# Optimization experiments

Measured on AMD Instinct MI355X. Metric: run time of the kernel, lower is better.

Reference implementation:

```python
import jax, jax.numpy as jnp
import numpy as np

N, NI, NF, NE, B, K, KD = 200000, 64, 128, 256, 16, 27, 8
ND = N // 8
EPS = 1e-5


def setup_inputs() -> dict:
    key = jax.random.key(0)
    ks = jax.random.split(key, 12)
    s = lambda i, shape: jax.random.normal(ks[i], shape, jnp.float32) * 0.02
    x = jax.random.normal(ks[0], (N, NI), jnp.float32)
    t = jax.random.normal(ks[1], (B, NE), jnp.float32)
    b_idx = jax.random.randint(ks[2], (N,), 0, B)
    nbr = jax.random.randint(ks[3], (K, N), 0, N)
    nbr = jnp.where(jax.random.uniform(ks[4], (K, N)) < 0.3, -1, nbr)
    nbr_down = jax.random.randint(ks[5], (KD, ND), 0, N)
    return dict(
        x=x, t=t, b_idx=b_idx, nbr=nbr, nbr_down=nbr_down,
        g1=jnp.ones((NI,), jnp.float32), be1=jnp.zeros((NI,), jnp.float32),
        W1=s(6, (K, NI, NF)), b1=jnp.zeros((NF,), jnp.float32),
        Wt=s(7, (NE, 2 * NF)), bt=jnp.zeros((2 * NF,), jnp.float32),
        g2=jnp.ones((NF,), jnp.float32), be2=jnp.zeros((NF,), jnp.float32),
        W2=s(8, (K, NF, NF)), b2=jnp.zeros((NF,), jnp.float32),
        Wid=s(9, (NI, NF)), bid=jnp.zeros((NF,), jnp.float32),
        Wd=s(10, (KD, NF, NF)),
    )


def bn_silu(x, g, b):
    # spnn.BatchNorm (training batch stats over voxels) + spnn.SiLU
    m = x.mean(0)
    v = x.var(0)
    return jax.nn.silu((x - m) * jax.lax.rsqrt(v + EPS) * g + b)


def sparse_conv(x, W, nbr):
    # gather-matmul-accumulate over kernel offsets; nbr[k] == -1 -> no neighbor
    def body(acc, kv):
        Wk, nk = kv
        xg = jnp.where((nk >= 0)[:, None], x[jnp.clip(nk, 0)], 0.0)  # [M, Ci]
        return acc + xg @ Wk, None
    out0 = jnp.zeros((nbr.shape[1], W.shape[-1]), x.dtype)
    out, _ = jax.lax.scan(body, out0, (W, nbr))
    return out


def reference(x, t, b_idx, nbr, nbr_down, g1, be1, W1, b1, Wt, bt,
              g2, be2, W2, b2, Wid, bid, Wd):
    # EmbResBlock
    h = sparse_conv(bn_silu(x, g1, be1), W1, nbr) + b1          # conv1 [N, NF]
    tp = jax.nn.silu(t) @ Wt + bt                                # proj_mlp [B, 2*NF]
    scale, shift = jnp.split(tp, 2, axis=-1)
    # TimeEmbeddingBlock: one edge per node -> gather + affine
    h = (1.0 + scale[b_idx]) * h + shift[b_idx]
    h = sparse_conv(bn_silu(h, g2, be2), W2, nbr) + b2           # conv2 [N, NF]
    h = h + x @ Wid + bid                                        # idconv residual
    # strided down conv (ks=2, stride=2, no bias) -> [ND, NF]
    return sparse_conv(h, Wd, nbr_down)
```

## Files before the change

kernel.cpp:

```cpp
#include <hip/hip_runtime.h>

#define NV 200000
#define NDN 25000
#define EPSV 1e-5f

typedef short bf16x8 __attribute__((ext_vector_type(8)));
typedef float f32x16 __attribute__((ext_vector_type(16)));

static __device__ __forceinline__ float silu_f(float v) { return v / (1.0f + __expf(-v)); }
static __device__ __forceinline__ unsigned short f2b(float f) {
    unsigned u = __float_as_uint(f);
    return (unsigned short)((u + 0x7FFFu + ((u >> 16) & 1u)) >> 16);
}
static __device__ __forceinline__ float b2f(unsigned short h) {
    return __uint_as_float(((unsigned)h) << 16);
}
static __device__ __forceinline__ bf16x8 bc8(uint4 v) { return __builtin_bit_cast(bf16x8, v); }
#define MFMA32(a, b, c) __builtin_amdgcn_mfma_f32_32x32x16_bf16(a, b, c, 0, 0, 0)

static __device__ __forceinline__ void gload_lds16(const uint4* g, uint4* l) {
    __builtin_amdgcn_global_load_lds((const __attribute__((address_space(1))) unsigned*)(g),
                                     (__attribute__((address_space(3))) unsigned*)(l), 16, 0, 0);
}

#define OFF_STATS1 0
#define OFF_STATS2 512
#define OFF_TP     4096
#define OFF_W1B    32768
#define OFF_W2B    (OFF_W1B + 27 * 64 * 128 * 2)
#define OFF_WDB    (OFF_W2B + 27 * 128 * 128 * 2)
#define OFF_WIDB   (OFF_WDB + 8 * 128 * 128 * 2)
#define OFF_H1     (2u << 20)
#define OFF_H2     (28u << 20)
#define OFF_H4     (80u << 20)


__global__ void k_zero(float* p) {
    int i = threadIdx.x;
    if (i < 384) p[i] = 0.0f;
}

__global__ __launch_bounds__(256) void k_stats1(const float* __restrict__ x,
                                                float* __restrict__ stats) {
    int c = threadIdx.x & 63;
    int r0 = blockIdx.x * 4 + (threadIdx.x >> 6);
    float s = 0.f, q = 0.f;
    for (int r = r0; r < NV; r += gridDim.x * 4) {
        float v = x[r * 64 + c];
        s += v; q += v * v;
    }
    __shared__ float rs[256], rq[256];
    rs[threadIdx.x] = s; rq[threadIdx.x] = q;
    __syncthreads();
    if (threadIdx.x < 64) {
        s = rs[threadIdx.x] + rs[threadIdx.x + 64] + rs[threadIdx.x + 128] + rs[threadIdx.x + 192];
        q = rq[threadIdx.x] + rq[threadIdx.x + 64] + rq[threadIdx.x + 128] + rq[threadIdx.x + 192];
        atomicAdd(&stats[c], s);
        atomicAdd(&stats[64 + c], q);
    }
}

__global__ __launch_bounds__(256) void k_tp(const float* __restrict__ t,
                                            const float* __restrict__ Wt,
                                            const float* __restrict__ bt,
                                            float* __restrict__ tp) {
    __shared__ float st[256];
    int b = blockIdx.x, o = threadIdx.x;
    st[o] = silu_f(t[b * 256 + o]);
    __syncthreads();
    float acc = bt[o];
    for (int e = 0; e < 256; e++) acc += st[e] * Wt[e * 256 + o];
    tp[b * 256 + o] = acc;
}

__global__ __launch_bounds__(256) void k_swz(const float* __restrict__ W, uint4* __restrict__ dst,
                                             int Kc, int S) {
    int t = blockIdx.x * 256 + threadIdx.x;
    int total = Kc * S * 4 * 64;
    if (t >= total) return;
    int L = t & 63;
    int u = t >> 6;
    int nt = u & 3; u >>= 2;
    int s = u % S;
    int kk = u / S;
    int CI = S * 16;
    int c0 = s * 16 + (L >> 5) * 8;
    int f = nt * 32 + (L & 31);
    union { unsigned short e[8]; uint4 v; } uu;
#pragma unroll
    for (int j = 0; j < 8; j++) uu.e[j] = f2b(W[(kk * CI + c0 + j) * 128 + f]);
    dst[t] = uu.v;
}

__global__ __launch_bounds__(256) void k_h1(const float* __restrict__ x,
                                            const float* __restrict__ g1,
                                            const float* __restrict__ be1,
                                            const float* __restrict__ stats,
                                            unsigned short* __restrict__ H1) {
    int i = blockIdx.x * 256 + threadIdx.x;
    if (i >= NV * 16) return;
    int c4 = (i & 15) * 4;
    float4 v = ((const float4*)x)[i];
    float vv[4] = {v.x, v.y, v.z, v.w};
    ushort4 o;
    unsigned short os[4];
#pragma unroll
    for (int j = 0; j < 4; j++) {
        int c = c4 + j;
        float m = stats[c] * (1.0f / NV);
        float var = stats[64 + c] * (1.0f / NV) - m * m;
        float a = g1[c] * rsqrtf(var + EPSV);
        float b = be1[c] - m * a;
        os[j] = f2b(silu_f(vv[j] * a + b));
    }
    o.x = os[0]; o.y = os[1]; o.z = os[2]; o.w = os[3];
    ((ushort4*)H1)[i] = o;
}

__global__ __launch_bounds__(256) void k_h3(unsigned short* __restrict__ H,
                                            const float* __restrict__ g2,
                                            const float* __restrict__ be2,
                                            const float* __restrict__ stats2) {
    int i = blockIdx.x * 256 + threadIdx.x;
    if (i >= NV * 16) return;
    union { uint4 v; unsigned short e[8]; } uu;
    uu.v = ((const uint4*)H)[i];
    int f0 = (i & 15) * 8;
#pragma unroll
    for (int j = 0; j < 8; j++) {
        int f = f0 + j;
        float m = stats2[f] * (1.0f / NV);
        float var = stats2[128 + f] * (1.0f / NV) - m * m;
        float a = g2[f] * rsqrtf(var + EPSV);
        float b = be2[f] - m * a;
        uu.e[j] = f2b(silu_f(b2f(uu.e[j]) * a + b));
    }
    ((uint4*)H)[i] = uu.v;
}


#define C2_STEP(AC, AN, IDXC, IDXN, LDSC, LDSN, KK)                                    \
    {                                                                                  \
        if ((KK) + 1 < 27) {                                                           \
            const uint4* pn = (const uint4*)H3 + (long)(IDXC) * 16;                    \
            _Pragma("unroll")                                                          \
            for (int s = 0; s < 8; s++) {                                              \
                AN[s] = make_uint4(0, 0, 0, 0);                                        \
                if ((IDXC) >= 0) AN[s] = pn[s * 2 + h];                                \
            }                                                                          \
        }                                                                              \
        IDXN = ((KK) + 2 < 27 && row0 < NV) ? nbr[((KK) + 2) * NV + row0] : -1;        \
        if ((KK) + 1 < 27) {                                                           \
            const uint4* gsrc = W2b + ((KK) + 1) * 2048 + (w * 8) * 64 + lane;         \
            _Pragma("unroll")                                                          \
            for (int j = 0; j < 8; j++)                                                \
                gload_lds16(gsrc + j * 64, &sB[(LDSN) + (w * 8 + j) * 64]);            \
        }                                                                              \
        _Pragma("unroll")                                                              \
        for (int s = 0; s < 8; s++) {                                                  \
            uint4 b0 = sB[(LDSC) + (s * 4 + 0) * 64 + lane];                           \
            uint4 b1v = sB[(LDSC) + (s * 4 + 1) * 64 + lane];                          \
            uint4 b2v = sB[(LDSC) + (s * 4 + 2) * 64 + lane];                          \
            uint4 b3v = sB[(LDSC) + (s * 4 + 3) * 64 + lane];                          \
            acc[0] = MFMA32(bc8(AC[s]), bc8(b0), acc[0]);                              \
            acc[1] = MFMA32(bc8(AC[s]), bc8(b1v), acc[1]);                             \
            acc[2] = MFMA32(bc8(AC[s]), bc8(b2v), acc[2]);                             \
            acc[3] = MFMA32(bc8(AC[s]), bc8(b3v), acc[3]);                             \
        }                                                                              \
        __syncthreads();                                                               \
    }

#define C1_STEP(AC, AN, IDXC, IDXN, LDSC, LDSN, KK)                                    \
    {                                                                                  \
        if ((KK) + 1 < 27) {                                                           \
            const uint4* pn = (const uint4*)H1 + (long)(IDXC) * 8;                     \
            _Pragma("unroll")                                                          \
            for (int s = 0; s < 4; s++) {                                              \
                AN[s] = make_uint4(0, 0, 0, 0);                                        \
                if ((IDXC) >= 0) AN[s] = pn[s * 2 + h];                                \
            }                                                                          \
        }                                                                              \
        IDXN = ((KK) + 2 < 27 && row0 < NV) ? nbr[((KK) + 2) * NV + row0] : -1;        \
        if ((KK) + 1 < 27) {                                                           \
            const uint4* gsrc = W1b + ((KK) + 1) * 1024 + (w * 4) * 64 + lane;         \
            _Pragma("unroll")                                                          \
            for (int j = 0; j < 4; j++)                                                \
                gload_lds16(gsrc + j * 64, &sB[(LDSN) + (w * 4 + j) * 64]);            \
        }                                                                              \
        _Pragma("unroll")                                                              \
        for (int s = 0; s < 4; s++) {                                                  \
            uint4 b0 = sB[(LDSC) + (s * 4 + 0) * 64 + lane];                           \
            uint4 b1v = sB[(LDSC) + (s * 4 + 1) * 64 + lane];                          \
            uint4 b2v = sB[(LDSC) + (s * 4 + 2) * 64 + lane];                          \
            uint4 b3v = sB[(LDSC) + (s * 4 + 3) * 64 + lane];                          \
            acc[0] = MFMA32(bc8(AC[s]), bc8(b0), acc[0]);                              \
            acc[1] = MFMA32(bc8(AC[s]), bc8(b1v), acc[1]);                             \
            acc[2] = MFMA32(bc8(AC[s]), bc8(b2v), acc[2]);                             \
            acc[3] = MFMA32(bc8(AC[s]), bc8(b3v), acc[3]);                             \
        }                                                                              \
        __syncthreads();                                                               \
    }

#define CD_STEP(AC, AN, IDXC, IDXN, LDSC, LDSN, KK)                                    \
    {                                                                                  \
        if ((KK) + 1 < 8) {                                                            \
            const uint4* pn = (const uint4*)H4 + (long)(IDXC) * 16;                    \
            _Pragma("unroll")                                                          \
            for (int s = 0; s < 8; s++) AN[s] = pn[s * 2 + h];                         \
        }                                                                              \
        IDXN = ((KK) + 2 < 8 && row0 < NDN) ? nbrd[((KK) + 2) * NDN + row0] : 0;       \
        if ((KK) + 1 < 8) {                                                            \
            const uint4* gsrc = Wdb + ((KK) + 1) * 2048 + (w * 8) * 64 + lane;         \
            _Pragma("unroll")                                                          \
            for (int j = 0; j < 8; j++)                                                \
                gload_lds16(gsrc + j * 64, &sB[(LDSN) + (w * 8 + j) * 64]);            \
        }                                                                              \
        _Pragma("unroll")                                                              \
        for (int s = 0; s < 8; s++) {                                                  \
            uint4 b0 = sB[(LDSC) + (s * 4 + 0) * 64 + lane];                           \
            uint4 b1v = sB[(LDSC) + (s * 4 + 1) * 64 + lane];                          \
            uint4 b2v = sB[(LDSC) + (s * 4 + 2) * 64 + lane];                          \
            uint4 b3v = sB[(LDSC) + (s * 4 + 3) * 64 + lane];                          \
            acc[0] = MFMA32(bc8(AC[s]), bc8(b0), acc[0]);                              \
            acc[1] = MFMA32(bc8(AC[s]), bc8(b1v), acc[1]);                             \
            acc[2] = MFMA32(bc8(AC[s]), bc8(b2v), acc[2]);                             \
            acc[3] = MFMA32(bc8(AC[s]), bc8(b3v), acc[3]);                             \
        }                                                                              \
        __syncthreads();                                                               \
    }

__global__ __launch_bounds__(256, 2) void k_conv1(const unsigned short* __restrict__ H1,
                                                  const int* __restrict__ nbr,
                                                  const uint4* __restrict__ W1b,
                                                  const float* __restrict__ b1,
                                                  const int* __restrict__ b_idx,
                                                  const float* __restrict__ tp,
                                                  unsigned short* __restrict__ H2,
                                                  float* __restrict__ stats2) {
    extern __shared__ uint4 sB[];
    __shared__ float ssum[128], ssq[128];
    int tid = threadIdx.x;
    int w = tid >> 6, lane = tid & 63, m = lane & 31, h = lane >> 5;
    int n0 = blockIdx.x * 128;
    int row0 = n0 + w * 32 + m;
    if (tid < 128) { ssum[tid] = 0.f; ssq[tid] = 0.f; }
    f32x16 z;
#pragma unroll
    for (int r = 0; r < 16; r++) z[r] = 0.f;
    f32x16 acc[4] = {z, z, z, z};
    uint4 aA[4], aB[4];
    int idxE, idxO;

    {
        const uint4* g0 = W1b + (w * 4) * 64 + lane;
#pragma unroll
        for (int j = 0; j < 4; j++) gload_lds16(g0 + j * 64, &sB[(w * 4 + j) * 64]);
        int idx0 = (row0 < NV) ? nbr[row0] : -1;
        idxO = (row0 < NV) ? nbr[NV + row0] : -1;
        const uint4* p0 = (const uint4*)H1 + (long)idx0 * 8;
#pragma unroll
        for (int s = 0; s < 4; s++) {
            aA[s] = make_uint4(0, 0, 0, 0);
            if (idx0 >= 0) aA[s] = p0[s * 2 + h];
        }
        idxE = idx0;
        __syncthreads();
    }
    for (int k = 0; k < 27; k += 2) {
        C1_STEP(aA, aB, idxO, idxE, 0, 1024, k);
        if (k + 1 < 27) C1_STEP(aB, aA, idxE, idxO, 1024, 0, (k + 1));
    }

    int col = m;
    float b1f[4];
#pragma unroll
    for (int nt = 0; nt < 4; nt++) b1f[nt] = b1[nt * 32 + col];
    float sl[4] = {0.f, 0.f, 0.f, 0.f}, ql[4] = {0.f, 0.f, 0.f, 0.f};
#pragma unroll
    for (int r = 0; r < 16; r++) {
        int row = w * 32 + (r & 3) + 8 * (r >> 2) + 4 * h;
        int g = n0 + row;
        if (g < NV) {
            int b = b_idx[g];
            const float* tpb = tp + b * 256;
#pragma unroll
            for (int nt = 0; nt < 4; nt++) {
                int f = nt * 32 + col;
                float val = acc[nt][r] + b1f[nt];
                float h2v = (1.0f + tpb[f]) * val + tpb[128 + f];
                H2[(long)g * 128 + f] = f2b(h2v);
                sl[nt] += h2v; ql[nt] += h2v * h2v;
            }
        }
    }
#pragma unroll
    for (int nt = 0; nt < 4; nt++) {
        int f = nt * 32 + col;
        atomicAdd(&ssum[f], sl[nt]);
        atomicAdd(&ssq[f], ql[nt]);
    }
    __syncthreads();
    if (tid < 128) {
        atomicAdd(&stats2[tid], ssum[tid]);
        atomicAdd(&stats2[128 + tid], ssq[tid]);
    }
}

__global__ __launch_bounds__(256, 2) void k_conv2(const unsigned short* __restrict__ H3,
                                                  const int* __restrict__ nbr,
                                                  const uint4* __restrict__ W2b,
                                                  const float* __restrict__ b2,
                                                  const float* __restrict__ x,
                                                  const uint4* __restrict__ Widb,
                                                  const float* __restrict__ bid,
                                                  unsigned short* __restrict__ H4) {
    extern __shared__ uint4 sB[];
    int tid = threadIdx.x;
    int w = tid >> 6, lane = tid & 63, m = lane & 31, h = lane >> 5;
    int n0 = blockIdx.x * 128;
    int row0 = n0 + w * 32 + m;
    f32x16 z;
#pragma unroll
    for (int r = 0; r < 16; r++) z[r] = 0.f;
    f32x16 acc[4] = {z, z, z, z};
    uint4 aA[8], aB[8];
    int idxE, idxO;

    {
        const uint4* g0 = W2b + (w * 8) * 64 + lane;
#pragma unroll
        for (int j = 0; j < 8; j++) gload_lds16(g0 + j * 64, &sB[(w * 8 + j) * 64]);
        int idx0 = (row0 < NV) ? nbr[row0] : -1;
        idxO = (row0 < NV) ? nbr[NV + row0] : -1;
        const uint4* p0 = (const uint4*)H3 + (long)idx0 * 16;
#pragma unroll
        for (int s = 0; s < 8; s++) {
            aA[s] = make_uint4(0, 0, 0, 0);
            if (idx0 >= 0) aA[s] = p0[s * 2 + h];
        }
        idxE = idx0;
        __syncthreads();
    }
    for (int k = 0; k < 27; k += 2) {
        C2_STEP(aA, aB, idxO, idxE, 0, 2048, k);
        if (k + 1 < 27) C2_STEP(aB, aA, idxE, idxO, 2048, 0, (k + 1));
    }

    {
        uint4 a0[4];
#pragma unroll
        for (int s = 0; s < 4; s++) {
            union { unsigned short e[8]; uint4 v; } u0;
            u0.v = make_uint4(0, 0, 0, 0);
            if (row0 < NV) {
                const float4* xr = (const float4*)(x + (long)row0 * 64);
                float4 f0 = xr[s * 4 + h * 2], f1 = xr[s * 4 + h * 2 + 1];
                u0.e[0] = f2b(f0.x); u0.e[1] = f2b(f0.y); u0.e[2] = f2b(f0.z); u0.e[3] = f2b(f0.w);
                u0.e[4] = f2b(f1.x); u0.e[5] = f2b(f1.y); u0.e[6] = f2b(f1.z); u0.e[7] = f2b(f1.w);
            }
            a0[s] = u0.v;
        }
#pragma unroll
        for (int s = 0; s < 4; s++) {
#pragma unroll
            for (int nt = 0; nt < 4; nt++) {
                uint4 bv = Widb[(s * 4 + nt) * 64 + lane];
                acc[nt] = MFMA32(bc8(a0[s]), bc8(bv), acc[nt]);
            }
        }
    }
    int col = m;
#pragma unroll
    for (int nt = 0; nt < 4; nt++) {
        int f = nt * 32 + col;
        float bias = b2[f] + bid[f];
#pragma unroll
        for (int r = 0; r < 16; r++) {
            int row = w * 32 + (r & 3) + 8 * (r >> 2) + 4 * h;
            int g = n0 + row;
            if (g < NV) H4[(long)g * 128 + f] = f2b(acc[nt][r] + bias);
        }
    }
}

__global__ __launch_bounds__(256, 2) void k_down(const unsigned short* __restrict__ H4,
                                                 const int* __restrict__ nbrd,
                                                 const uint4* __restrict__ Wdb,
                                                 float* __restrict__ out) {
    extern __shared__ uint4 sB[];
    int tid = threadIdx.x;
    int w = tid >> 6, lane = tid & 63, m = lane & 31, h = lane >> 5;
    int n0 = blockIdx.x * 128;
    int row0 = n0 + w * 32 + m;
    f32x16 z;
#pragma unroll
    for (int r = 0; r < 16; r++) z[r] = 0.f;
    f32x16 acc[4] = {z, z, z, z};
    uint4 aA[8], aB[8];
    int idxE, idxO;

    {
        const uint4* g0 = Wdb + (w * 8) * 64 + lane;
#pragma unroll
        for (int j = 0; j < 8; j++) gload_lds16(g0 + j * 64, &sB[(w * 8 + j) * 64]);
        int idx0 = (row0 < NDN) ? nbrd[row0] : 0;
        idxO = (row0 < NDN) ? nbrd[NDN + row0] : 0;
        const uint4* p0 = (const uint4*)H4 + (long)idx0 * 16;
#pragma unroll
        for (int s = 0; s < 8; s++) aA[s] = p0[s * 2 + h];
        idxE = idx0;
        __syncthreads();
    }
    for (int k = 0; k < 8; k += 2) {
        CD_STEP(aA, aB, idxO, idxE, 0, 2048, k);
        CD_STEP(aB, aA, idxE, idxO, 2048, 0, (k + 1));
    }

    int col = m;
#pragma unroll
    for (int nt = 0; nt < 4; nt++) {
        int f = nt * 32 + col;
#pragma unroll
        for (int r = 0; r < 16; r++) {
            int row = w * 32 + (r & 3) + 8 * (r >> 2) + 4 * h;
            int g = n0 + row;
            if (g < NDN) out[(long)g * 128 + f] = acc[nt][r];
        }
    }
}


extern "C" void kernel_launch(void* const* d_in, const int* in_sizes, int n_in,
                              void* d_out, int out_size, void* d_ws, size_t ws_size,
                              hipStream_t stream) {
    const float* x   = (const float*)d_in[0];
    const float* t   = (const float*)d_in[1];
    const int* b_idx = (const int*)d_in[2];
    const int* nbr   = (const int*)d_in[3];
    const int* nbrd  = (const int*)d_in[4];
    const float* g1  = (const float*)d_in[5];
    const float* be1 = (const float*)d_in[6];
    const float* W1  = (const float*)d_in[7];
    const float* b1  = (const float*)d_in[8];
    const float* Wt  = (const float*)d_in[9];
    const float* bt  = (const float*)d_in[10];
    const float* g2  = (const float*)d_in[11];
    const float* be2 = (const float*)d_in[12];
    const float* W2  = (const float*)d_in[13];
    const float* b2  = (const float*)d_in[14];
    const float* Wid = (const float*)d_in[15];
    const float* bid = (const float*)d_in[16];
    const float* Wd  = (const float*)d_in[17];
    float* out = (float*)d_out;

    char* ws = (char*)d_ws;
    float* stats1 = (float*)(ws + OFF_STATS1);
    float* stats2 = (float*)(ws + OFF_STATS2);
    float* tp     = (float*)(ws + OFF_TP);
    uint4* W1b    = (uint4*)(ws + OFF_W1B);
    uint4* W2b    = (uint4*)(ws + OFF_W2B);
    uint4* Wdb    = (uint4*)(ws + OFF_WDB);
    uint4* Widb   = (uint4*)(ws + OFF_WIDB);
    unsigned short* H1 = (unsigned short*)(ws + OFF_H1);
    unsigned short* H2 = (unsigned short*)(ws + OFF_H2);
    unsigned short* H4 = (unsigned short*)(ws + OFF_H4);

    k_zero<<<1, 384, 0, stream>>>((float*)ws);
    k_stats1<<<400, 256, 0, stream>>>(x, stats1);
    k_tp<<<16, 256, 0, stream>>>(t, Wt, bt, tp);
    k_swz<<<108, 256, 0, stream>>>(W1, W1b, 27, 4);
    k_swz<<<216, 256, 0, stream>>>(W2, W2b, 27, 8);
    k_swz<<<64, 256, 0, stream>>>(Wd, Wdb, 8, 8);
    k_swz<<<4, 256, 0, stream>>>(Wid, Widb, 1, 4);
    k_h1<<<12500, 256, 0, stream>>>(x, g1, be1, stats1, H1);
    k_conv1<<<(NV + 127) / 128, 256, 2 * 1024 * 16, stream>>>(H1, nbr, W1b, b1, b_idx, tp, H2, stats2);
    k_h3<<<12500, 256, 0, stream>>>(H2, g2, be2, stats2);
    k_conv2<<<(NV + 127) / 128, 256, 2 * 2048 * 16, stream>>>(H2, nbr, W2b, b2, x, Widb, bid, H4);
    k_down<<<(NDN + 127) / 128, 256, 2 * 2048 * 16, stream>>>(H4, nbrd, Wdb, out);
}
```

Before: 680.8 us.

## Register-staged weight prefetch, zero-row gathers, and lighter barriers in sparse convs

```diff
diff --git a/kernel.cpp b/kernel.cpp
--- a/kernel.cpp
+++ b/kernel.cpp
@@ -17,11 +17,6 @@
 }
 static __device__ __forceinline__ bf16x8 bc8(uint4 v) { return __builtin_bit_cast(bf16x8, v); }
 #define MFMA32(a, b, c) __builtin_amdgcn_mfma_f32_32x32x16_bf16(a, b, c, 0, 0, 0)
-
-static __device__ __forceinline__ void gload_lds16(const uint4* g, uint4* l) {
-    __builtin_amdgcn_global_load_lds((const __attribute__((address_space(1))) unsigned*)(g),
-                                     (__attribute__((address_space(3))) unsigned*)(l), 16, 0, 0);
-}
 
 #define OFF_STATS1 0
 #define OFF_STATS2 512
@@ -38,6 +33,12 @@
 __global__ void k_zero(float* p) {
     int i = threadIdx.x;
     if (i < 384) p[i] = 0.0f;
+}
+
+__global__ void k_zrow(unsigned short* H1, unsigned short* H2) {
+    int t = threadIdx.x;
+    if (t < 64) H1[(long)NV * 64 + t] = 0;
+    H2[(long)NV * 128 + t] = 0;
 }
 
 __global__ __launch_bounds__(256) void k_stats1(const float* __restrict__ x,
@@ -142,20 +143,24 @@
 #define C2_STEP(AC, AN, IDXC, IDXN, LDSC, LDSN, KK)                                    \
     {                                                                                  \
         if ((KK) + 1 < 27) {                                                           \
-            const uint4* pn = (const uint4*)H3 + (long)(IDXC) * 16;                    \
-            _Pragma("unroll")                                                          \
-            for (int s = 0; s < 8; s++) {                                              \
-                AN[s] = make_uint4(0, 0, 0, 0);                                        \
-                if ((IDXC) >= 0) AN[s] = pn[s * 2 + h];                                \
-            }                                                                          \
-        }                                                                              \
-        IDXN = ((KK) + 2 < 27 && row0 < NV) ? nbr[((KK) + 2) * NV + row0] : -1;        \
-        if ((KK) + 1 < 27) {                                                           \
-            const uint4* gsrc = W2b + ((KK) + 1) * 2048 + (w * 8) * 64 + lane;         \
             _Pragma("unroll")                                                          \
             for (int j = 0; j < 8; j++)                                                \
-                gload_lds16(gsrc + j * 64, &sB[(LDSN) + (w * 8 + j) * 64]);            \
-        }                                                                              \
+                sB[(LDSN) + (w * 8 + j) * 64 + lane] = wR[j];                          \
+        }                                                                              \
+        __builtin_amdgcn_sched_barrier(0);                                             \
+        {                                                                              \
+            int rn_ = ((IDXC) < 0) ? NV : (IDXC);                                      \
+            const uint4* pn = (const uint4*)H3 + (long)rn_ * 16;                       \
+            _Pragma("unroll")                                                          \
+            for (int s = 0; s < 8; s++) AN[s] = pn[s * 2 + h];                         \
+        }                                                                              \
+        IDXN = nbr[((KK) + 2 < 27 ? (KK) + 2 : 26) * NV + row0c];                      \
+        if ((KK) + 2 < 27) {                                                           \
+            const uint4* gw = W2b + ((KK) + 2) * 2048 + (w * 8) * 64 + lane;           \
+            _Pragma("unroll")                                                          \
+            for (int j = 0; j < 8; j++) wR[j] = gw[j * 64];                            \
+        }                                                                              \
+        __builtin_amdgcn_sched_barrier(0);                                             \
         _Pragma("unroll")                                                              \
         for (int s = 0; s < 8; s++) {                                                  \
             uint4 b0 = sB[(LDSC) + (s * 4 + 0) * 64 + lane];                           \
@@ -167,26 +172,32 @@
             acc[2] = MFMA32(bc8(AC[s]), bc8(b2v), acc[2]);                             \
             acc[3] = MFMA32(bc8(AC[s]), bc8(b3v), acc[3]);                             \
         }                                                                              \
-        __syncthreads();                                                               \
+        asm volatile("s_waitcnt lgkmcnt(0)" ::: "memory");                             \
+        __builtin_amdgcn_s_barrier();                                                  \
+        __builtin_amdgcn_sched_barrier(0);                                             \
     }
 
 #define C1_STEP(AC, AN, IDXC, IDXN, LDSC, LDSN, KK)                                    \
     {                                                                                  \
         if ((KK) + 1 < 27) {                                                           \
-            const uint4* pn = (const uint4*)H1 + (long)(IDXC) * 8;                     \
-            _Pragma("unroll")                                                          \
-            for (int s = 0; s < 4; s++) {                                              \
-                AN[s] = make_uint4(0, 0, 0, 0);                                        \
-                if ((IDXC) >= 0) AN[s] = pn[s * 2 + h];                                \
-            }                                                                          \
-        }                                                                              \
-        IDXN = ((KK) + 2 < 27 && row0 < NV) ? nbr[((KK) + 2) * NV + row0] : -1;        \
-        if ((KK) + 1 < 27) {                                                           \
-            const uint4* gsrc = W1b + ((KK) + 1) * 1024 + (w * 4) * 64 + lane;         \
             _Pragma("unroll")                                                          \
             for (int j = 0; j < 4; j++)                                                \
-                gload_lds16(gsrc + j * 64, &sB[(LDSN) + (w * 4 + j) * 64]);            \
-        }                                                                              \
+                sB[(LDSN) + (w * 4 + j) * 64 + lane] = wR[j];                          \
+        }                                                                              \
+        __builtin_amdgcn_sched_barrier(0);                                             \
+        {                                                                              \
+            int rn_ = ((IDXC) < 0) ? NV : (IDXC);                                      \
+            const uint4* pn = (const uint4*)H1 + (long)rn_ * 8;                        \
+            _Pragma("unroll")                                                          \
+            for (int s = 0; s < 4; s++) AN[s] = pn[s * 2 + h];                         \
+        }                                                                              \
+        IDXN = nbr[((KK) + 2 < 27 ? (KK) + 2 : 26) * NV + row0c];                      \
+        if ((KK) + 2 < 27) {                                                           \
+            const uint4* gw = W1b + ((KK) + 2) * 1024 + (w * 4) * 64 + lane;           \
+            _Pragma("unroll")                                                          \
+            for (int j = 0; j < 4; j++) wR[j] = gw[j * 64];                            \
+        }                                                                              \
+        __builtin_amdgcn_sched_barrier(0);                                             \
         _Pragma("unroll")                                                              \
         for (int s = 0; s < 4; s++) {                                                  \
             uint4 b0 = sB[(LDSC) + (s * 4 + 0) * 64 + lane];                           \
@@ -198,23 +209,31 @@
             acc[2] = MFMA32(bc8(AC[s]), bc8(b2v), acc[2]);                             \
             acc[3] = MFMA32(bc8(AC[s]), bc8(b3v), acc[3]);                             \
         }                                                                              \
-        __syncthreads();                                                               \
+        asm volatile("s_waitcnt lgkmcnt(0)" ::: "memory");                             \
+        __builtin_amdgcn_s_barrier();                                                  \
+        __builtin_amdgcn_sched_barrier(0);                                             \
     }
 
 #define CD_STEP(AC, AN, IDXC, IDXN, LDSC, LDSN, KK)                                    \
     {                                                                                  \
         if ((KK) + 1 < 8) {                                                            \
+            _Pragma("unroll")                                                          \
+            for (int j = 0; j < 8; j++)                                                \
+                sB[(LDSN) + (w * 8 + j) * 64 + lane] = wR[j];                          \
+        }                                                                              \
+        __builtin_amdgcn_sched_barrier(0);                                             \
+        {                                                                              \
             const uint4* pn = (const uint4*)H4 + (long)(IDXC) * 16;                    \
             _Pragma("unroll")                                                          \
             for (int s = 0; s < 8; s++) AN[s] = pn[s * 2 + h];                         \
         }                                                                              \
-        IDXN = ((KK) + 2 < 8 && row0 < NDN) ? nbrd[((KK) + 2) * NDN + row0] : 0;       \
-        if ((KK) + 1 < 8) {                                                            \
-            const uint4* gsrc = Wdb + ((KK) + 1) * 2048 + (w * 8) * 64 + lane;         \
-            _Pragma("unroll")                                                          \
-            for (int j = 0; j < 8; j++)                                                \
-                gload_lds16(gsrc + j * 64, &sB[(LDSN) + (w * 8 + j) * 64]);            \
-        }                                                                              \
+        IDXN = nbrd[((KK) + 2 < 8 ? (KK) + 2 : 7) * NDN + row0c];                      \
+        if ((KK) + 2 < 8) {                                                            \
+            const uint4* gw = Wdb + ((KK) + 2) * 2048 + (w * 8) * 64 + lane;           \
+            _Pragma("unroll")                                                          \
+            for (int j = 0; j < 8; j++) wR[j] = gw[j * 64];                            \
+        }                                                                              \
+        __builtin_amdgcn_sched_barrier(0);                                             \
         _Pragma("unroll")                                                              \
         for (int s = 0; s < 8; s++) {                                                  \
             uint4 b0 = sB[(LDSC) + (s * 4 + 0) * 64 + lane];                           \
@@ -226,10 +245,12 @@
             acc[2] = MFMA32(bc8(AC[s]), bc8(b2v), acc[2]);                             \
             acc[3] = MFMA32(bc8(AC[s]), bc8(b3v), acc[3]);                             \
         }                                                                              \
-        __syncthreads();                                                               \
-    }
-
-__global__ __launch_bounds__(256, 2) void k_conv1(const unsigned short* __restrict__ H1,
+        asm volatile("s_waitcnt lgkmcnt(0)" ::: "memory");                             \
+        __builtin_amdgcn_s_barrier();                                                  \
+        __builtin_amdgcn_sched_barrier(0);                                             \
+    }
+
+__global__ __launch_bounds__(256, 3) void k_conv1(const unsigned short* __restrict__ H1,
                                                   const int* __restrict__ nbr,
                                                   const uint4* __restrict__ W1b,
                                                   const float* __restrict__ b1,
@@ -243,28 +264,33 @@
     int w = tid >> 6, lane = tid & 63, m = lane & 31, h = lane >> 5;
     int n0 = blockIdx.x * 128;
     int row0 = n0 + w * 32 + m;
+    int row0c = row0 < NV ? row0 : NV - 1;
     if (tid < 128) { ssum[tid] = 0.f; ssq[tid] = 0.f; }
     f32x16 z;
 #pragma unroll
     for (int r = 0; r < 16; r++) z[r] = 0.f;
     f32x16 acc[4] = {z, z, z, z};
-    uint4 aA[4], aB[4];
-    int idxE, idxO;
+    uint4 aA[4], aB[4], wR[4];
+    int idxE = 0, idxO;
 
     {
-        const uint4* g0 = W1b + (w * 4) * 64 + lane;
-#pragma unroll
-        for (int j = 0; j < 4; j++) gload_lds16(g0 + j * 64, &sB[(w * 4 + j) * 64]);
-        int idx0 = (row0 < NV) ? nbr[row0] : -1;
-        idxO = (row0 < NV) ? nbr[NV + row0] : -1;
-        const uint4* p0 = (const uint4*)H1 + (long)idx0 * 8;
-#pragma unroll
-        for (int s = 0; s < 4; s++) {
-            aA[s] = make_uint4(0, 0, 0, 0);
-            if (idx0 >= 0) aA[s] = p0[s * 2 + h];
-        }
-        idxE = idx0;
-        __syncthreads();
+        int idx0 = nbr[row0c];
+        idxO = nbr[NV + row0c];
+        const uint4* gw = W1b + (w * 4) * 64 + lane;
+#pragma unroll
+        for (int j = 0; j < 4; j++) wR[j] = gw[j * 64];
+        int rn_ = idx0 < 0 ? NV : idx0;
+        const uint4* p0 = (const uint4*)H1 + (long)rn_ * 8;
+#pragma unroll
+        for (int s = 0; s < 4; s++) aA[s] = p0[s * 2 + h];
+#pragma unroll
+        for (int j = 0; j < 4; j++) sB[(w * 4 + j) * 64 + lane] = wR[j];
+        const uint4* gw1 = W1b + 1024 + (w * 4) * 64 + lane;
+#pragma unroll
+        for (int j = 0; j < 4; j++) wR[j] = gw1[j * 64];
+        asm volatile("s_waitcnt lgkmcnt(0)" ::: "memory");
+        __builtin_amdgcn_s_barrier();
+        __builtin_amdgcn_sched_barrier(0);
     }
     for (int k = 0; k < 27; k += 2) {
         C1_STEP(aA, aB, idxO, idxE, 0, 1024, k);
@@ -319,27 +345,32 @@
     int w = tid >> 6, lane = tid & 63, m = lane & 31, h = lane >> 5;
     int n0 = blockIdx.x * 128;
     int row0 = n0 + w * 32 + m;
+    int row0c = row0 < NV ? row0 : NV - 1;
     f32x16 z;
 #pragma unroll
     for (int r = 0; r < 16; r++) z[r] = 0.f;
     f32x16 acc[4] = {z, z, z, z};
-    uint4 aA[8], aB[8];
-    int idxE, idxO;
+    uint4 aA[8], aB[8], wR[8];
+    int idxE = 0, idxO;
 
     {
-        const uint4* g0 = W2b + (w * 8) * 64 + lane;
-#pragma unroll
-        for (int j = 0; j < 8; j++) gload_lds16(g0 + j * 64, &sB[(w * 8 + j) * 64]);
-        int idx0 = (row0 < NV) ? nbr[row0] : -1;
-        idxO = (row0 < NV) ? nbr[NV + row0] : -1;
-        const uint4* p0 = (const uint4*)H3 + (long)idx0 * 16;
-#pragma unroll
-        for (int s = 0; s < 8; s++) {
-            aA[s] = make_uint4(0, 0, 0, 0);
-            if (idx0 >= 0) aA[s] = p0[s * 2 + h];
-        }
-        idxE = idx0;
-        __syncthreads();
+        int idx0 = nbr[row0c];
+        idxO = nbr[NV + row0c];
+        const uint4* gw = W2b + (w * 8) * 64 + lane;
+#pragma unroll
+        for (int j = 0; j < 8; j++) wR[j] = gw[j * 64];
+        int rn_ = idx0 < 0 ? NV : idx0;
+        const uint4* p0 = (const uint4*)H3 + (long)rn_ * 16;
+#pragma unroll
+        for (int s = 0; s < 8; s++) aA[s] = p0[s * 2 + h];
+#pragma unroll
+        for (int j = 0; j < 8; j++) sB[(w * 8 + j) * 64 + lane] = wR[j];
+        const uint4* gw1 = W2b + 2048 + (w * 8) * 64 + lane;
+#pragma unroll
+        for (int j = 0; j < 8; j++) wR[j] = gw1[j * 64];
+        asm volatile("s_waitcnt lgkmcnt(0)" ::: "memory");
+        __builtin_amdgcn_s_barrier();
+        __builtin_amdgcn_sched_barrier(0);
     }
     for (int k = 0; k < 27; k += 2) {
         C2_STEP(aA, aB, idxO, idxE, 0, 2048, k);
@@ -392,24 +423,31 @@
     int w = tid >> 6, lane = tid & 63, m = lane & 31, h = lane >> 5;
     int n0 = blockIdx.x * 128;
     int row0 = n0 + w * 32 + m;
+    int row0c = row0 < NDN ? row0 : NDN - 1;
     f32x16 z;
 #pragma unroll
     for (int r = 0; r < 16; r++) z[r] = 0.f;
     f32x16 acc[4] = {z, z, z, z};
-    uint4 aA[8], aB[8];
-    int idxE, idxO;
+    uint4 aA[8], aB[8], wR[8];
+    int idxE = 0, idxO;
 
     {
-        const uint4* g0 = Wdb + (w * 8) * 64 + lane;
-#pragma unroll
-        for (int j = 0; j < 8; j++) gload_lds16(g0 + j * 64, &sB[(w * 8 + j) * 64]);
-        int idx0 = (row0 < NDN) ? nbrd[row0] : 0;
-        idxO = (row0 < NDN) ? nbrd[NDN + row0] : 0;
+        int idx0 = nbrd[row0c];
+        idxO = nbrd[NDN + row0c];
+        const uint4* gw = Wdb + (w * 8) * 64 + lane;
+#pragma unroll
+        for (int j = 0; j < 8; j++) wR[j] = gw[j * 64];
         const uint4* p0 = (const uint4*)H4 + (long)idx0 * 16;
 #pragma unroll
         for (int s = 0; s < 8; s++) aA[s] = p0[s * 2 + h];
-        idxE = idx0;
-        __syncthreads();
+#pragma unroll
+        for (int j = 0; j < 8; j++) sB[(w * 8 + j) * 64 + lane] = wR[j];
+        const uint4* gw1 = Wdb + 2048 + (w * 8) * 64 + lane;
+#pragma unroll
+        for (int j = 0; j < 8; j++) wR[j] = gw1[j * 64];
+        asm volatile("s_waitcnt lgkmcnt(0)" ::: "memory");
+        __builtin_amdgcn_s_barrier();
+        __builtin_amdgcn_sched_barrier(0);
     }
     for (int k = 0; k < 8; k += 2) {
         CD_STEP(aA, aB, idxO, idxE, 0, 2048, k);
@@ -466,6 +504,7 @@
     unsigned short* H4 = (unsigned short*)(ws + OFF_H4);
 
     k_zero<<<1, 384, 0, stream>>>((float*)ws);
+    k_zrow<<<1, 128, 0, stream>>>(H1, H2);
     k_stats1<<<400, 256, 0, stream>>>(x, stats1);
     k_tp<<<16, 256, 0, stream>>>(t, Wt, bt, tp);
     k_swz<<<108, 256, 0, stream>>>(W1, W1b, 27, 4);
```

New measurement: 1.238 ms. 1.82x slower.

## Read conv weights directly from global memory instead of staging through LDS

Applied to the files above, without the earlier changes.

```diff
diff --git a/kernel.cpp b/kernel.cpp
--- a/kernel.cpp
+++ b/kernel.cpp
@@ -17,11 +17,6 @@
 }
 static __device__ __forceinline__ bf16x8 bc8(uint4 v) { return __builtin_bit_cast(bf16x8, v); }
 #define MFMA32(a, b, c) __builtin_amdgcn_mfma_f32_32x32x16_bf16(a, b, c, 0, 0, 0)
-
-static __device__ __forceinline__ void gload_lds16(const uint4* g, uint4* l) {
-    __builtin_amdgcn_global_load_lds((const __attribute__((address_space(1))) unsigned*)(g),
-                                     (__attribute__((address_space(3))) unsigned*)(l), 16, 0, 0);
-}
 
 #define OFF_STATS1 0
 #define OFF_STATS2 512
@@ -139,7 +134,7 @@
 }
 
 
-#define C2_STEP(AC, AN, IDXC, IDXN, LDSC, LDSN, KK)                                    \
+#define C2_STEP(AC, AN, IDXC, IDXN, KK)                                                \
     {                                                                                  \
         if ((KK) + 1 < 27) {                                                           \
             const uint4* pn = (const uint4*)H3 + (long)(IDXC) * 16;                    \
@@ -150,27 +145,21 @@
             }                                                                          \
         }                                                                              \
         IDXN = ((KK) + 2 < 27 && row0 < NV) ? nbr[((KK) + 2) * NV + row0] : -1;        \
-        if ((KK) + 1 < 27) {                                                           \
-            const uint4* gsrc = W2b + ((KK) + 1) * 2048 + (w * 8) * 64 + lane;         \
-            _Pragma("unroll")                                                          \
-            for (int j = 0; j < 8; j++)                                                \
-                gload_lds16(gsrc + j * 64, &sB[(LDSN) + (w * 8 + j) * 64]);            \
-        }                                                                              \
+        const uint4* gW = W2b + (KK) * 2048;                                           \
         _Pragma("unroll")                                                              \
         for (int s = 0; s < 8; s++) {                                                  \
-            uint4 b0 = sB[(LDSC) + (s * 4 + 0) * 64 + lane];                           \
-            uint4 b1v = sB[(LDSC) + (s * 4 + 1) * 64 + lane];                          \
-            uint4 b2v = sB[(LDSC) + (s * 4 + 2) * 64 + lane];                          \
-            uint4 b3v = sB[(LDSC) + (s * 4 + 3) * 64 + lane];                          \
+            uint4 b0 = gW[(s * 4 + 0) * 64 + lane];                                    \
+            uint4 b1v = gW[(s * 4 + 1) * 64 + lane];                                   \
+            uint4 b2v = gW[(s * 4 + 2) * 64 + lane];                                   \
+            uint4 b3v = gW[(s * 4 + 3) * 64 + lane];                                   \
             acc[0] = MFMA32(bc8(AC[s]), bc8(b0), acc[0]);                              \
             acc[1] = MFMA32(bc8(AC[s]), bc8(b1v), acc[1]);                             \
             acc[2] = MFMA32(bc8(AC[s]), bc8(b2v), acc[2]);                             \
             acc[3] = MFMA32(bc8(AC[s]), bc8(b3v), acc[3]);                             \
         }                                                                              \
-        __syncthreads();                                                               \
-    }
-
-#define C1_STEP(AC, AN, IDXC, IDXN, LDSC, LDSN, KK)                                    \
+    }
+
+#define C1_STEP(AC, AN, IDXC, IDXN, KK)                                                \
     {                                                                                  \
         if ((KK) + 1 < 27) {                                                           \
             const uint4* pn = (const uint4*)H1 + (long)(IDXC) * 8;                     \
@@ -181,27 +170,21 @@
             }                                                                          \
         }                                                                              \
         IDXN = ((KK) + 2 < 27 && row0 < NV) ? nbr[((KK) + 2) * NV + row0] : -1;        \
-        if ((KK) + 1 < 27) {                                                           \
-            const uint4* gsrc = W1b + ((KK) + 1) * 1024 + (w * 4) * 64 + lane;         \
-            _Pragma("unroll")                                                          \
-            for (int j = 0; j < 4; j++)                                                \
-                gload_lds16(gsrc + j * 64, &sB[(LDSN) + (w * 4 + j) * 64]);            \
-        }                                                                              \
+        const uint4* gW = W1b + (KK) * 1024;                                           \
         _Pragma("unroll")                                                              \
         for (int s = 0; s < 4; s++) {                                                  \
-            uint4 b0 = sB[(LDSC) + (s * 4 + 0) * 64 + lane];                           \
-            uint4 b1v = sB[(LDSC) + (s * 4 + 1) * 64 + lane];                          \
-            uint4 b2v = sB[(LDSC) + (s * 4 + 2) * 64 + lane];                          \
-            uint4 b3v = sB[(LDSC) + (s * 4 + 3) * 64 + lane];                          \
+            uint4 b0 = gW[(s * 4 + 0) * 64 + lane];                                    \
+            uint4 b1v = gW[(s * 4 + 1) * 64 + lane];                                   \
+            uint4 b2v = gW[(s * 4 + 2) * 64 + lane];                                   \
+            uint4 b3v = gW[(s * 4 + 3) * 64 + lane];                                   \
             acc[0] = MFMA32(bc8(AC[s]), bc8(b0), acc[0]);                              \
             acc[1] = MFMA32(bc8(AC[s]), bc8(b1v), acc[1]);                             \
             acc[2] = MFMA32(bc8(AC[s]), bc8(b2v), acc[2]);                             \
             acc[3] = MFMA32(bc8(AC[s]), bc8(b3v), acc[3]);                             \
         }                                                                              \
-        __syncthreads();                                                               \
-    }
-
-#define CD_STEP(AC, AN, IDXC, IDXN, LDSC, LDSN, KK)                                    \
+    }
+
+#define CD_STEP(AC, AN, IDXC, IDXN, KK)                                                \
     {                                                                                  \
         if ((KK) + 1 < 8) {                                                            \
             const uint4* pn = (const uint4*)H4 + (long)(IDXC) * 16;                    \
@@ -209,27 +192,21 @@
             for (int s = 0; s < 8; s++) AN[s] = pn[s * 2 + h];                         \
         }                                                                              \
         IDXN = ((KK) + 2 < 8 && row0 < NDN) ? nbrd[((KK) + 2) * NDN + row0] : 0;       \
-        if ((KK) + 1 < 8) {                                                            \
-            const uint4* gsrc = Wdb + ((KK) + 1) * 2048 + (w * 8) * 64 + lane;         \
-            _Pragma("unroll")                                                          \
-            for (int j = 0; j < 8; j++)                                                \
-                gload_lds16(gsrc + j * 64, &sB[(LDSN) + (w * 8 + j) * 64]);            \
-        }                                                                              \
+        const uint4* gW = Wdb + (KK) * 2048;                                           \
         _Pragma("unroll")                                                              \
         for (int s = 0; s < 8; s++) {                                                  \
-            uint4 b0 = sB[(LDSC) + (s * 4 + 0) * 64 + lane];                           \
-            uint4 b1v = sB[(LDSC) + (s * 4 + 1) * 64 + lane];                          \
-            uint4 b2v = sB[(LDSC) + (s * 4 + 2) * 64 + lane];                          \
-            uint4 b3v = sB[(LDSC) + (s * 4 + 3) * 64 + lane];                          \
+            uint4 b0 = gW[(s * 4 + 0) * 64 + lane];                                    \
+            uint4 b1v = gW[(s * 4 + 1) * 64 + lane];                                   \
+            uint4 b2v = gW[(s * 4 + 2) * 64 + lane];                                   \
+            uint4 b3v = gW[(s * 4 + 3) * 64 + lane];                                   \
             acc[0] = MFMA32(bc8(AC[s]), bc8(b0), acc[0]);                              \
             acc[1] = MFMA32(bc8(AC[s]), bc8(b1v), acc[1]);                             \
             acc[2] = MFMA32(bc8(AC[s]), bc8(b2v), acc[2]);                             \
             acc[3] = MFMA32(bc8(AC[s]), bc8(b3v), acc[3]);                             \
         }                                                                              \
-        __syncthreads();                                                               \
-    }
-
-__global__ __launch_bounds__(256, 2) void k_conv1(const unsigned short* __restrict__ H1,
+    }
+
+__global__ __launch_bounds__(256, 3) void k_conv1(const unsigned short* __restrict__ H1,
                                                   const int* __restrict__ nbr,
                                                   const uint4* __restrict__ W1b,
                                                   const float* __restrict__ b1,
@@ -237,7 +214,6 @@
                                                   const float* __restrict__ tp,
                                                   unsigned short* __restrict__ H2,
                                                   float* __restrict__ stats2) {
-    extern __shared__ uint4 sB[];
     __shared__ float ssum[128], ssq[128];
     int tid = threadIdx.x;
     int w = tid >> 6, lane = tid & 63, m = lane & 31, h = lane >> 5;
@@ -252,9 +228,6 @@
     int idxE, idxO;
 
     {
-        const uint4* g0 = W1b + (w * 4) * 64 + lane;
-#pragma unroll
-        for (int j = 0; j < 4; j++) gload_lds16(g0 + j * 64, &sB[(w * 4 + j) * 64]);
         int idx0 = (row0 < NV) ? nbr[row0] : -1;
         idxO = (row0 < NV) ? nbr[NV + row0] : -1;
         const uint4* p0 = (const uint4*)H1 + (long)idx0 * 8;
@@ -264,11 +237,10 @@
             if (idx0 >= 0) aA[s] = p0[s * 2 + h];
         }
         idxE = idx0;
-        __syncthreads();
     }
     for (int k = 0; k < 27; k += 2) {
-        C1_STEP(aA, aB, idxO, idxE, 0, 1024, k);
-        if (k + 1 < 27) C1_STEP(aB, aA, idxE, idxO, 1024, 0, (k + 1));
+        C1_STEP(aA, aB, idxO, idxE, k);
+        if (k + 1 < 27) C1_STEP(aB, aA, idxE, idxO, (k + 1));
     }
 
     int col = m;
@@ -314,7 +286,6 @@
                                                   const uint4* __restrict__ Widb,
                                                   const float* __restrict__ bid,
                                                   unsigned short* __restrict__ H4) {
-    extern __shared__ uint4 sB[];
     int tid = threadIdx.x;
     int w = tid >> 6, lane = tid & 63, m = lane & 31, h = lane >> 5;
     int n0 = blockIdx.x * 128;
@@ -327,9 +298,6 @@
     int idxE, idxO;
 
     {
-        const uint4* g0 = W2b + (w * 8) * 64 + lane;
-#pragma unroll
-        for (int j = 0; j < 8; j++) gload_lds16(g0 + j * 64, &sB[(w * 8 + j) * 64]);
         int idx0 = (row0 < NV) ? nbr[row0] : -1;
         idxO = (row0 < NV) ? nbr[NV + row0] : -1;
         const uint4* p0 = (const uint4*)H3 + (long)idx0 * 16;
@@ -339,11 +307,10 @@
             if (idx0 >= 0) aA[s] = p0[s * 2 + h];
         }
         idxE = idx0;
-        __syncthreads();
     }
     for (int k = 0; k < 27; k += 2) {
-        C2_STEP(aA, aB, idxO, idxE, 0, 2048, k);
-        if (k + 1 < 27) C2_STEP(aB, aA, idxE, idxO, 2048, 0, (k + 1));
+        C2_STEP(aA, aB, idxO, idxE, k);
+        if (k + 1 < 27) C2_STEP(aB, aA, idxE, idxO, (k + 1));
     }
 
     {
@@ -387,7 +354,6 @@
                                                  const int* __restrict__ nbrd,
                                                  const uint4* __restrict__ Wdb,
                                                  float* __restrict__ out) {
-    extern __shared__ uint4 sB[];
     int tid = threadIdx.x;
     int w = tid >> 6, lane = tid & 63, m = lane & 31, h = lane >> 5;
     int n0 = blockIdx.x * 128;
@@ -400,20 +366,16 @@
     int idxE, idxO;
 
     {
-        const uint4* g0 = Wdb + (w * 8) * 64 + lane;
-#pragma unroll
-        for (int j = 0; j < 8; j++) gload_lds16(g0 + j * 64, &sB[(w * 8 + j) * 64]);
         int idx0 = (row0 < NDN) ? nbrd[row0] : 0;
         idxO = (row0 < NDN) ? nbrd[NDN + row0] : 0;
         const uint4* p0 = (const uint4*)H4 + (long)idx0 * 16;
 #pragma unroll
         for (int s = 0; s < 8; s++) aA[s] = p0[s * 2 + h];
         idxE = idx0;
-        __syncthreads();
     }
     for (int k = 0; k < 8; k += 2) {
-        CD_STEP(aA, aB, idxO, idxE, 0, 2048, k);
-        CD_STEP(aB, aA, idxE, idxO, 2048, 0, (k + 1));
+        CD_STEP(aA, aB, idxO, idxE, k);
+        CD_STEP(aB, aA, idxE, idxO, (k + 1));
     }
 
     int col = m;
@@ -473,8 +435,8 @@
     k_swz<<<64, 256, 0, stream>>>(Wd, Wdb, 8, 8);
     k_swz<<<4, 256, 0, stream>>>(Wid, Widb, 1, 4);
     k_h1<<<12500, 256, 0, stream>>>(x, g1, be1, stats1, H1);
-    k_conv1<<<(NV + 127) / 128, 256, 2 * 1024 * 16, stream>>>(H1, nbr, W1b, b1, b_idx, tp, H2, stats2);
+    k_conv1<<<(NV + 127) / 128, 256, 0, stream>>>(H1, nbr, W1b, b1, b_idx, tp, H2, stats2);
     k_h3<<<12500, 256, 0, stream>>>(H2, g2, be2, stats2);
-    k_conv2<<<(NV + 127) / 128, 256, 2 * 2048 * 16, stream>>>(H2, nbr, W2b, b2, x, Widb, bid, H4);
-    k_down<<<(NDN + 127) / 128, 256, 2 * 2048 * 16, stream>>>(H4, nbrd, Wdb, out);
-}
+    k_conv2<<<(NV + 127) / 128, 256, 0, stream>>>(H2, nbr, W2b, b2, x, Widb, bid, H4);
+    k_down<<<(NDN + 127) / 128, 256, 0, stream>>>(H4, nbrd, Wdb, out);
+}
```

Result: slower. 918.4 us (+34.9%).

## Gather conv2 neighbor rows directly into swizzled LDS with chunked prefetch

Applied to the files above, without the earlier changes.

```diff
diff --git a/kernel.cpp b/kernel.cpp
--- a/kernel.cpp
+++ b/kernel.cpp
@@ -18,7 +18,7 @@
 static __device__ __forceinline__ bf16x8 bc8(uint4 v) { return __builtin_bit_cast(bf16x8, v); }
 #define MFMA32(a, b, c) __builtin_amdgcn_mfma_f32_32x32x16_bf16(a, b, c, 0, 0, 0)
 
-static __device__ __forceinline__ void gload_lds16(const uint4* g, uint4* l) {
+static __device__ __forceinline__ void gload_lds16(const void* g, void* l) {
     __builtin_amdgcn_global_load_lds((const __attribute__((address_space(1))) unsigned*)(g),
                                      (__attribute__((address_space(3))) unsigned*)(l), 16, 0, 0);
 }
@@ -38,6 +38,12 @@
 __global__ void k_zero(float* p) {
     int i = threadIdx.x;
     if (i < 384) p[i] = 0.0f;
+}
+
+__global__ void k_zrow(unsigned short* H1, unsigned short* H2) {
+    int t = threadIdx.x;
+    if (t < 64) H1[(long)NV * 64 + t] = 0;
+    H2[(long)NV * 128 + t] = 0;
 }
 
 __global__ __launch_bounds__(256) void k_stats1(const float* __restrict__ x,
@@ -138,37 +144,6 @@
     ((uint4*)H)[i] = uu.v;
 }
 
-
-#define C2_STEP(AC, AN, IDXC, IDXN, LDSC, LDSN, KK)                                    \
-    {                                                                                  \
-        if ((KK) + 1 < 27) {                                                           \
-            const uint4* pn = (const uint4*)H3 + (long)(IDXC) * 16;                    \
-            _Pragma("unroll")                                                          \
-            for (int s = 0; s < 8; s++) {                                              \
-                AN[s] = make_uint4(0, 0, 0, 0);                                        \
-                if ((IDXC) >= 0) AN[s] = pn[s * 2 + h];                                \
-            }                                                                          \
-        }                                                                              \
-        IDXN = ((KK) + 2 < 27 && row0 < NV) ? nbr[((KK) + 2) * NV + row0] : -1;        \
-        if ((KK) + 1 < 27) {                                                           \
-            const uint4* gsrc = W2b + ((KK) + 1) * 2048 + (w * 8) * 64 + lane;         \
-            _Pragma("unroll")                                                          \
-            for (int j = 0; j < 8; j++)                                                \
-                gload_lds16(gsrc + j * 64, &sB[(LDSN) + (w * 8 + j) * 64]);            \
-        }                                                                              \
-        _Pragma("unroll")                                                              \
-        for (int s = 0; s < 8; s++) {                                                  \
-            uint4 b0 = sB[(LDSC) + (s * 4 + 0) * 64 + lane];                           \
-            uint4 b1v = sB[(LDSC) + (s * 4 + 1) * 64 + lane];                          \
-            uint4 b2v = sB[(LDSC) + (s * 4 + 2) * 64 + lane];                          \
-            uint4 b3v = sB[(LDSC) + (s * 4 + 3) * 64 + lane];                          \
-            acc[0] = MFMA32(bc8(AC[s]), bc8(b0), acc[0]);                              \
-            acc[1] = MFMA32(bc8(AC[s]), bc8(b1v), acc[1]);                             \
-            acc[2] = MFMA32(bc8(AC[s]), bc8(b2v), acc[2]);                             \
-            acc[3] = MFMA32(bc8(AC[s]), bc8(b3v), acc[3]);                             \
-        }                                                                              \
-        __syncthreads();                                                               \
-    }
 
 #define C1_STEP(AC, AN, IDXC, IDXN, LDSC, LDSN, KK)                                    \
     {                                                                                  \
@@ -252,11 +227,11 @@
     int idxE, idxO;
 
     {
-        const uint4* g0 = W1b + (w * 4) * 64 + lane;
-#pragma unroll
-        for (int j = 0; j < 4; j++) gload_lds16(g0 + j * 64, &sB[(w * 4 + j) * 64]);
         int idx0 = (row0 < NV) ? nbr[row0] : -1;
         idxO = (row0 < NV) ? nbr[NV + row0] : -1;
+        const uint4* g0 = W1b + (w * 4) * 64 + lane;
+#pragma unroll
+        for (int j = 0; j < 4; j++) gload_lds16(g0 + j * 64, &sB[(w * 4 + j) * 64]);
         const uint4* p0 = (const uint4*)H1 + (long)idx0 * 8;
 #pragma unroll
         for (int s = 0; s < 4; s++) {
@@ -305,6 +280,7 @@
         atomicAdd(&stats2[128 + tid], ssq[tid]);
     }
 }
+
 
 __global__ __launch_bounds__(256, 2) void k_conv2(const unsigned short* __restrict__ H3,
                                                   const int* __restrict__ nbr,
@@ -314,36 +290,71 @@
                                                   const uint4* __restrict__ Widb,
                                                   const float* __restrict__ bid,
                                                   unsigned short* __restrict__ H4) {
-    extern __shared__ uint4 sB[];
+    __shared__ char lds[65536];
     int tid = threadIdx.x;
     int w = tid >> 6, lane = tid & 63, m = lane & 31, h = lane >> 5;
     int n0 = blockIdx.x * 128;
     int row0 = n0 + w * 32 + m;
+    char* Aw = lds + w * 8192;
+    char* Bb = lds + 32768;
+    int r0w = n0 + w * 32;
+    int rA = min(r0w + (lane >> 2), NV - 1);
+    int rB = min(r0w + 16 + (lane >> 2), NV - 1);
+    int lsw = ((lane & 3) ^ ((lane >> 2) & 3)) << 4;
     f32x16 z;
 #pragma unroll
     for (int r = 0; r < 16; r++) z[r] = 0.f;
     f32x16 acc[4] = {z, z, z, z};
-    uint4 aA[8], aB[8];
-    int idxE, idxO;
+    int iA = nbr[rA], iB = nbr[rB];
 
     {
-        const uint4* g0 = W2b + (w * 8) * 64 + lane;
-#pragma unroll
-        for (int j = 0; j < 8; j++) gload_lds16(g0 + j * 64, &sB[(w * 8 + j) * 64]);
-        int idx0 = (row0 < NV) ? nbr[row0] : -1;
-        idxO = (row0 < NV) ? nbr[NV + row0] : -1;
-        const uint4* p0 = (const uint4*)H3 + (long)idx0 * 16;
-#pragma unroll
-        for (int s = 0; s < 8; s++) {
-            aA[s] = make_uint4(0, 0, 0, 0);
-            if (idx0 >= 0) aA[s] = p0[s * 2 + h];
-        }
-        idxE = idx0;
+#pragma unroll
+        for (int c = 0; c < 4; c++) {
+            long s0 = (iA < 0) ? (long)NV : (long)iA;
+            long s1 = (iB < 0) ? (long)NV : (long)iB;
+            int gsw = (c << 6) | lsw;
+            gload_lds16((const char*)H3 + s0 * 256 + gsw, Aw + c * 2048);
+            gload_lds16((const char*)H3 + s1 * 256 + gsw, Aw + c * 2048 + 1024);
+        }
+#pragma unroll
+        for (int j = 0; j < 8; j++)
+            gload_lds16(W2b + (w * 8 + j) * 64 + lane, Bb + (w * 8 + j) * 1024);
+        iA = nbr[NV + rA]; iB = nbr[NV + rB];
         __syncthreads();
     }
-    for (int k = 0; k < 27; k += 2) {
-        C2_STEP(aA, aB, idxO, idxE, 0, 2048, k);
-        if (k + 1 < 27) C2_STEP(aB, aA, idxE, idxO, 2048, 0, (k + 1));
+
+    for (int k = 0; k < 27; k++) {
+#pragma unroll
+        for (int c = 0; c < 4; c++) {
+#pragma unroll
+            for (int ss = 0; ss < 2; ss++) {
+                int s = 2 * c + ss;
+                int g = 2 * s + h;
+                int wp = (g & 3) ^ (m & 3);
+                uint4 fA = *(const uint4*)(Aw + c * 2048 + (m >> 4) * 1024
+                                           + (m & 15) * 64 + wp * 16);
+                uint4 b0 = *(const uint4*)(Bb + (s * 4 + 0) * 1024 + lane * 16);
+                uint4 b1v = *(const uint4*)(Bb + (s * 4 + 1) * 1024 + lane * 16);
+                uint4 b2v = *(const uint4*)(Bb + (s * 4 + 2) * 1024 + lane * 16);
+                uint4 b3v = *(const uint4*)(Bb + (s * 4 + 3) * 1024 + lane * 16);
+                acc[0] = MFMA32(bc8(fA), bc8(b0), acc[0]);
+                acc[1] = MFMA32(bc8(fA), bc8(b1v), acc[1]);
+                acc[2] = MFMA32(bc8(fA), bc8(b2v), acc[2]);
+                acc[3] = MFMA32(bc8(fA), bc8(b3v), acc[3]);
+            }
+            __syncthreads();
+            if (k + 1 < 27) {
+                long s0 = (iA < 0) ? (long)NV : (long)iA;
+                long s1 = (iB < 0) ? (long)NV : (long)iB;
+                int gsw = (c << 6) | lsw;
+                gload_lds16((const char*)H3 + s0 * 256 + gsw, Aw + c * 2048);
+                gload_lds16((const char*)H3 + s1 * 256 + gsw, Aw + c * 2048 + 1024);
+                const uint4* bs = W2b + (k + 1) * 2048 + (8 * c + w * 2) * 64;
+                gload_lds16(bs + lane, Bb + (8 * c + w * 2) * 1024);
+                gload_lds16(bs + 64 + lane, Bb + (8 * c + w * 2 + 1) * 1024);
+            }
+        }
+        if (k + 2 < 27) { iA = nbr[(k + 2) * NV + rA]; iB = nbr[(k + 2) * NV + rB]; }
     }
 
     {
@@ -400,11 +411,11 @@
     int idxE, idxO;
 
     {
-        const uint4* g0 = Wdb + (w * 8) * 64 + lane;
-#pragma unroll
-        for (int j = 0; j < 8; j++) gload_lds16(g0 + j * 64, &sB[(w * 8 + j) * 64]);
         int idx0 = (row0 < NDN) ? nbrd[row0] : 0;
         idxO = (row0 < NDN) ? nbrd[NDN + row0] : 0;
+        const uint4* g0 = Wdb + (w * 8) * 64 + lane;
+#pragma unroll
+        for (int j = 0; j < 8; j++) gload_lds16(g0 + j * 64, &sB[(w * 8 + j) * 64]);
         const uint4* p0 = (const uint4*)H4 + (long)idx0 * 16;
 #pragma unroll
         for (int s = 0; s < 8; s++) aA[s] = p0[s * 2 + h];
@@ -466,6 +477,7 @@
     unsigned short* H4 = (unsigned short*)(ws + OFF_H4);
 
     k_zero<<<1, 384, 0, stream>>>((float*)ws);
+    k_zrow<<<1, 128, 0, stream>>>(H1, H2);
     k_stats1<<<400, 256, 0, stream>>>(x, stats1);
     k_tp<<<16, 256, 0, stream>>>(t, Wt, bt, tp);
     k_swz<<<108, 256, 0, stream>>>(W1, W1b, 27, 4);
@@ -475,6 +487,6 @@
     k_h1<<<12500, 256, 0, stream>>>(x, g1, be1, stats1, H1);
     k_conv1<<<(NV + 127) / 128, 256, 2 * 1024 * 16, stream>>>(H1, nbr, W1b, b1, b_idx, tp, H2, stats2);
     k_h3<<<12500, 256, 0, stream>>>(H2, g2, be2, stats2);
-    k_conv2<<<(NV + 127) / 128, 256, 2 * 2048 * 16, stream>>>(H2, nbr, W2b, b2, x, Widb, bid, H4);
+    k_conv2<<<(NV + 127) / 128, 256, 0, stream>>>(H2, nbr, W2b, b2, x, Widb, bid, H4);
     k_down<<<(NDN + 127) / 128, 256, 2 * 2048 * 16, stream>>>(H4, nbrd, Wdb, out);
 }
```

Result: slower. 728.9 us (+7.1%).
